# Performance work log

Hardware: AMD Instinct MI355X
Metric: run time of the kernel (lower is better)

## Reference

```python
import jax, jax.numpy as jnp
import numpy as np

B, C, H, W, D = 1, 128, 64, 64, 64
CQ = C // 8


def setup_inputs() -> dict:
    key = jax.random.key(0)
    ks = jax.random.split(key, 6)
    s = 0.05
    return {
        "x": jax.random.normal(ks[0], (B, C, H, W, D), jnp.float32),
        "y": jax.random.normal(ks[1], (B, C, H, W, D), jnp.float32),
        "Wq": jax.random.normal(ks[2], (CQ, C), jnp.float32) * s,
        "bq": jnp.zeros((CQ,), jnp.float32),
        "Wk": jax.random.normal(ks[3], (CQ, C), jnp.float32) * s,
        "bk": jnp.zeros((CQ,), jnp.float32),
        "Wv": jax.random.normal(ks[4], (C, C), jnp.float32) * s,
        "bv": jnp.zeros((C,), jnp.float32),
        # torch inits gamma to 0 (kills all attention grads); use a nonzero value
        "gamma": jax.random.normal(ks[5], (1,), jnp.float32),
    }


def _conv1x1(x, Wt, b):
    # 1x1x1 Conv3d == per-voxel linear over channels
    return jnp.einsum('bchwd,oc->bohwd', x, Wt) + b[None, :, None, None, None]


def _criss_cross(x, y, Wq, bq, Wk, bk, Wv, bv, gamma):
    Bs, Cs, Hs, Ws, Ds = x.shape
    Cq = Wq.shape[0]
    q = _conv1x1(x, Wq, bq)  # [B,Cq,H,W,D]
    k = _conv1x1(y, Wk, bk)  # [B,Cq,H,W,D]
    v = _conv1x1(x, Wv, bv)  # [B,C ,H,W,D]

    # exact transliteration of the torch permute/contiguous/view sequence
    qH = q.transpose(0, 3, 4, 1, 2).reshape(Bs * Ws * Ds, Cq, Hs).transpose(0, 2, 1)
    qW = q.transpose(0, 2, 4, 1, 3).reshape(Bs * Hs * Ds, Cq, Ws).transpose(0, 2, 1)
    qD = q.transpose(0, 2, 3, 1, 4).reshape(Bs * Hs * Ws, Cq, Ds).transpose(0, 2, 1)
    kH = k.transpose(0, 3, 4, 1, 2).reshape(Bs * Ws * Ds, Cq, Hs)
    kW = k.transpose(0, 2, 4, 1, 3).reshape(Bs * Hs * Ds, Cq, Ws)
    kD = k.transpose(0, 2, 3, 1, 4).reshape(Bs * Hs * Ws, Cq, Ds)
    vH = v.transpose(0, 3, 4, 1, 2).reshape(Bs * Ws * Ds, Cs, Hs)
    vW = v.transpose(0, 2, 4, 1, 3).reshape(Bs * Hs * Ds, Cs, Ws)
    vD = v.transpose(0, 2, 3, 1, 4).reshape(Bs * Hs * Ws, Cs, Ds)

    # INF(): -inf on the HxH diagonal, broadcast over the B*W*D batch
    inf_mask = jnp.where(jnp.eye(Hs, dtype=bool), -jnp.inf, 0.0)[None].astype(x.dtype)

    energy_H = (jnp.matmul(qH, kH) + inf_mask).reshape(Bs, Ws, Hs, Ds, Hs).transpose(0, 2, 1, 3, 4)
    energy_W = jnp.matmul(qW, kW).reshape(Bs, Hs, Ws, Ds, Ws)
    energy_D = jnp.matmul(qD, kD).reshape(Bs, Hs, Ws, Ds, Ds)

    # NOTE: original uses Softmax(dim=3) on the 5D concat -> softmax over the D axis
    concate = jax.nn.softmax(jnp.concatenate([energy_H, energy_W, energy_D], axis=4), axis=3)

    att_H = concate[..., 0:Hs].transpose(0, 2, 1, 3, 4).reshape(Bs * Ws * Ds, Hs, Hs)
    att_W = concate[..., Hs:Hs + Ws].reshape(Bs * Hs * Ds, Ws, Ws)
    att_D = concate[..., Hs + Ws:Hs + Ws + Ds].reshape(Bs * Hs * Ws, Ds, Ds)

    out_H = jnp.matmul(vH, att_H.transpose(0, 2, 1)).reshape(Bs, Ws, Cs, Hs, Ds).transpose(0, 2, 3, 1, 4)
    out_W = jnp.matmul(vW, att_W.transpose(0, 2, 1)).reshape(Bs, Hs, Cs, Ws, Ds).transpose(0, 2, 1, 3, 4)
    out_D = jnp.matmul(vD, att_D.transpose(0, 2, 1)).reshape(Bs, Hs, Cs, Ws, Ds).transpose(0, 2, 1, 3, 4)

    return gamma[0] * (out_H + out_W + out_D) + x


def reference(x, y, Wq, bq, Wk, bk, Wv, bv, gamma):
    return _criss_cross(x, y, Wq, bq, Wk, bk, Wv, bv, gamma)
```

## Files before the change

kernel.cpp:

```cpp
#include <hip/hip_runtime.h>

#define HWD 262144
#define WD  4096

typedef unsigned short bf16_t;
typedef unsigned short u16;
struct __align__(8) us4 { unsigned short x, y, z, w; };

typedef __bf16 bf16x8 __attribute__((ext_vector_type(8)));
typedef float  f32x4  __attribute__((ext_vector_type(4)));

__device__ inline float b2f(unsigned short u) {
    return __uint_as_float(((unsigned int)u) << 16);
}
__device__ inline unsigned short f2b(float f) {
    unsigned int u = __float_as_uint(f);
    u += 0x7fff + ((u >> 16) & 1);
    return (unsigned short)(u >> 16);
}

union FragU { us4 h[2]; bf16x8 v; };
__device__ inline bf16x8 ld8_a8(const u16* p) {
    FragU f; f.h[0] = *(const us4*)p; f.h[1] = *(const us4*)(p + 4); return f.v;
}
__device__ inline bf16x8 ld8_a16(const u16* p) {
    return *(const bf16x8*)p;
}

struct HL { bf16x8 h, l; };
__device__ inline HL split8(const float* w8) {
    FragU H, L;
    unsigned short hh[8], ll[8];
#pragma unroll
    for (int t = 0; t < 8; ++t) {
        hh[t] = f2b(w8[t]);
        ll[t] = f2b(w8[t] - b2f(hh[t]));
    }
    H.h[0].x = hh[0]; H.h[0].y = hh[1]; H.h[0].z = hh[2]; H.h[0].w = hh[3];
    H.h[1].x = hh[4]; H.h[1].y = hh[5]; H.h[1].z = hh[6]; H.h[1].w = hh[7];
    L.h[0].x = ll[0]; L.h[0].y = ll[1]; L.h[0].z = ll[2]; L.h[0].w = ll[3];
    L.h[1].x = ll[4]; L.h[1].y = ll[5]; L.h[1].z = ll[6]; L.h[1].w = ll[7];
    HL r; r.h = H.v; r.l = L.v; return r;
}

__global__ __launch_bounds__(512, 4) void conv_v_mfma(
    const float* __restrict__ x, const float* __restrict__ Wv,
    const float* __restrict__ bv, bf16_t* __restrict__ v)
{
    __shared__ __align__(16) u16 Xh[64][136];
    __shared__ __align__(16) u16 Xl[64][136];
    const int tid  = threadIdx.x;
    const int lane = tid & 63;
    const int wv   = tid >> 6;
    const int lg = lane >> 4, lr = lane & 15;
    const int n0 = blockIdx.x * 64;

    const int m0 = wv * 16;
    bf16x8 Ah[4], Al[4];
#pragma unroll
    for (int ks = 0; ks < 4; ++ks) {
        float w8[8];
        const float* wp = &Wv[(m0 + lr) * 128 + ks * 32 + lg * 8];
        *(float4*)&w8[0] = *(const float4*)wp;
        *(float4*)&w8[4] = *(const float4*)(wp + 4);
        HL hl = split8(w8);
        Ah[ks] = hl.h; Al[ks] = hl.l;
    }

#pragma unroll
    for (int gi = 0; gi < 2; ++gi) {
        const int g = wv + gi * 8;
        float v8[8];
#pragma unroll
        for (int s = 0; s < 8; ++s)
            v8[s] = x[(size_t)(g * 8 + s) * HWD + n0 + lane];
        HL hl = split8(v8);
        *(bf16x8*)&Xh[lane][g * 8] = hl.h;
        *(bf16x8*)&Xl[lane][g * 8] = hl.l;
    }
    __syncthreads();

    f32x4 acc[4];
#pragma unroll
    for (int ns = 0; ns < 4; ++ns) acc[ns] = (f32x4){0.f, 0.f, 0.f, 0.f};
#pragma unroll
    for (int ks = 0; ks < 4; ++ks) {
#pragma unroll
        for (int ns = 0; ns < 4; ++ns) {
            const bf16x8 Bh = ld8_a16(&Xh[ns * 16 + lr][ks * 32 + lg * 8]);
            const bf16x8 Bl = ld8_a16(&Xl[ns * 16 + lr][ks * 32 + lg * 8]);
            acc[ns] = __builtin_amdgcn_mfma_f32_16x16x32_bf16(Ah[ks], Bh, acc[ns], 0, 0, 0);
            acc[ns] = __builtin_amdgcn_mfma_f32_16x16x32_bf16(Ah[ks], Bl, acc[ns], 0, 0, 0);
            acc[ns] = __builtin_amdgcn_mfma_f32_16x16x32_bf16(Al[ks], Bh, acc[ns], 0, 0, 0);
        }
    }
#pragma unroll
    for (int ns = 0; ns < 4; ++ns)
#pragma unroll
        for (int r = 0; r < 4; ++r) {
            const int m = m0 + 4 * lg + r;
            v[(size_t)m * HWD + n0 + ns * 16 + lr] = f2b(acc[ns][r] + bv[m]);
        }
}

__global__ __launch_bounds__(256, 4) void conv_qk_mfma(
    const float* __restrict__ x, const float* __restrict__ y,
    const float* __restrict__ Wq, const float* __restrict__ bq,
    const float* __restrict__ Wk, const float* __restrict__ bk,
    bf16_t* __restrict__ q, bf16_t* __restrict__ k)
{
    __shared__ __align__(16) u16 Sh[2][32][136];
    __shared__ __align__(16) u16 Sl[2][32][136];
    const int tid  = threadIdx.x;
    const int lane = tid & 63;
    const int wv   = tid >> 6;
    const int lg = lane >> 4, lr = lane & 15;
    const int n0 = blockIdx.x * 32;

    const float* W    = (wv < 2) ? Wq : Wk;
    const float* bias = (wv < 2) ? bq : bk;
    bf16_t*      dst  = (wv < 2) ? q  : k;
    bf16x8 Ah[4], Al[4];
#pragma unroll
    for (int ks = 0; ks < 4; ++ks) {
        float w8[8];
        const float* wp = &W[lr * 128 + ks * 32 + lg * 8];
        *(float4*)&w8[0] = *(const float4*)wp;
        *(float4*)&w8[4] = *(const float4*)(wp + 4);
        HL hl = split8(w8);
        Ah[ks] = hl.h; Al[ks] = hl.l;
    }

    {
        const int n  = tid & 31;
        const int kb = (tid >> 5) * 16;
#pragma unroll
        for (int a = 0; a < 2; ++a) {
            const float* src = a ? y : x;
#pragma unroll
            for (int gg = 0; gg < 2; ++gg) {
                float v8[8];
#pragma unroll
                for (int s = 0; s < 8; ++s)
                    v8[s] = src[(size_t)(kb + gg * 8 + s) * HWD + n0 + n];
                HL hl = split8(v8);
                *(bf16x8*)&Sh[a][n][kb + gg * 8] = hl.h;
                *(bf16x8*)&Sl[a][n][kb + gg * 8] = hl.l;
            }
        }
    }
    __syncthreads();

    const int a  = wv >> 1;
    const int ns = wv & 1;
    f32x4 acc = (f32x4){0.f, 0.f, 0.f, 0.f};
#pragma unroll
    for (int ks = 0; ks < 4; ++ks) {
        const bf16x8 Bh = ld8_a16(&Sh[a][ns * 16 + lr][ks * 32 + lg * 8]);
        const bf16x8 Bl = ld8_a16(&Sl[a][ns * 16 + lr][ks * 32 + lg * 8]);
        acc = __builtin_amdgcn_mfma_f32_16x16x32_bf16(Ah[ks], Bh, acc, 0, 0, 0);
        acc = __builtin_amdgcn_mfma_f32_16x16x32_bf16(Ah[ks], Bl, acc, 0, 0, 0);
        acc = __builtin_amdgcn_mfma_f32_16x16x32_bf16(Al[ks], Bh, acc, 0, 0, 0);
    }
#pragma unroll
    for (int r = 0; r < 4; ++r) {
        const int m = 4 * lg + r;
        dst[(size_t)m * HWD + n0 + ns * 16 + lr] = f2b(acc[r] + bias[m]);
    }
}

__global__ __launch_bounds__(256) void t_wd_kernel(
    const bf16_t* __restrict__ src, bf16_t* __restrict__ dst)
{
    const int h = blockIdx.x, c = blockIdx.y;
    __shared__ bf16_t tile[64][68];
    const size_t base = (size_t)c * HWD + h * WD;
    const int tid = threadIdx.x;
#pragma unroll
    for (int i = 0; i < 4; ++i) {
        const int f = (tid + i * 256) * 4;
        const int w = f >> 6, d = f & 63;
        const us4 val = *(const us4*)&src[base + w * 64 + d];
        tile[w][d] = val.x; tile[w][d + 1] = val.y;
        tile[w][d + 2] = val.z; tile[w][d + 3] = val.w;
    }
    __syncthreads();
#pragma unroll
    for (int i = 0; i < 4; ++i) {
        const int f = (tid + i * 256) * 4;
        const int d = f >> 6, w0 = f & 63;
        us4 o; o.x = tile[w0][d]; o.y = tile[w0 + 1][d];
        o.z = tile[w0 + 2][d]; o.w = tile[w0 + 3][d];
        *(us4*)&dst[base + d * 64 + w0] = o;
    }
}

__global__ __launch_bounds__(256) void t_hd_kernel(
    const bf16_t* __restrict__ src, bf16_t* __restrict__ dst)
{
    const int w = blockIdx.x, c = blockIdx.y;
    __shared__ bf16_t tile[64][68];
    const size_t cb = (size_t)c * HWD;
    const int tid = threadIdx.x;
#pragma unroll
    for (int i = 0; i < 4; ++i) {
        const int f = (tid + i * 256) * 4;
        const int h = f >> 6, d0 = f & 63;
        const us4 val = *(const us4*)&src[cb + h * WD + w * 64 + d0];
        tile[h][d0] = val.x; tile[h][d0 + 1] = val.y;
        tile[h][d0 + 2] = val.z; tile[h][d0 + 3] = val.w;
    }
    __syncthreads();
#pragma unroll
    for (int i = 0; i < 4; ++i) {
        const int f = (tid + i * 256) * 4;
        const int d = f >> 6, h0 = f & 63;
        us4 o; o.x = tile[h0][d]; o.y = tile[h0 + 1][d];
        o.z = tile[h0 + 2][d]; o.w = tile[h0 + 3][d];
        *(us4*)&dst[cb + w * WD + d * 64 + h0] = o;
    }
}

template<bool MASK>
__device__ __forceinline__ void cc_phase(
    const u16* __restrict__ qp, const u16* __restrict__ kp,
    const u16* __restrict__ vp, const size_t base, const int tid,
    u16 (*Qt)[36], u16 (*Kt)[36], u16 (*Vs)[72],
    float (*EA)[68], u16 (*PB)[72], float (*red)[64], f32x4* acc)
{
    const int w  = tid >> 6;
    const int l  = tid & 63;
    const int lg = l >> 4, lr = l & 15;

    __syncthreads();
    us4 vreg[8];
#pragma unroll
    for (int i = 0; i < 8; ++i) {
        const int f = (tid + i * 256) * 4;
        vreg[i] = *(const us4*)&vp[(size_t)(f >> 6) * HWD + base + (f & 63)];
    }
    {
        const int j = tid & 63, c0 = (tid >> 6) * 4;
        const size_t gb = base + j;
        us4 qv, kv;
        qv.x = qp[(size_t)(c0 + 0) * HWD + gb];
        qv.y = qp[(size_t)(c0 + 1) * HWD + gb];
        qv.z = qp[(size_t)(c0 + 2) * HWD + gb];
        qv.w = qp[(size_t)(c0 + 3) * HWD + gb];
        kv.x = kp[(size_t)(c0 + 0) * HWD + gb];
        kv.y = kp[(size_t)(c0 + 1) * HWD + gb];
        kv.z = kp[(size_t)(c0 + 2) * HWD + gb];
        kv.w = kp[(size_t)(c0 + 3) * HWD + gb];
        *(us4*)&Qt[j][c0] = qv;
        *(us4*)&Kt[j][c0] = kv;
    }
    __syncthreads();
    {
        const bf16x8 bk = ld8_a8(&Kt[16 * w + lr][8 * lg]);
#pragma unroll
        for (int ti = 0; ti < 4; ++ti) {
            const bf16x8 aq = ld8_a8(&Qt[16 * ti + lr][8 * lg]);
            f32x4 e = {0.f, 0.f, 0.f, 0.f};
            e = __builtin_amdgcn_mfma_f32_16x16x32_bf16(aq, bk, e, 0, 0, 0);
#pragma unroll
            for (int r = 0; r < 4; ++r)
                EA[16 * ti + 4 * lg + r][16 * w + lr] = e[r];
        }
    }
    __syncthreads();
    {
        const int j = tid & 63, seg = tid >> 6;
        float vals[16];
        float m = -1e30f;
#pragma unroll
        for (int i = 0; i < 16; ++i) {
            float vv = EA[seg * 16 + i][j];
            if (MASK && (seg * 16 + i) == j) vv = -1e30f;
            vals[i] = vv; m = fmaxf(m, vv);
        }
        red[seg][j] = m;
        __syncthreads();
        m = fmaxf(fmaxf(red[0][j], red[1][j]), fmaxf(red[2][j], red[3][j]));
        float ss = 0.f;
#pragma unroll
        for (int i = 0; i < 16; ++i) { vals[i] = __expf(vals[i] - m); ss += vals[i]; }
        __syncthreads();
        red[seg][j] = ss;
        __syncthreads();
        ss = red[0][j] + red[1][j] + red[2][j] + red[3][j];
        const float inv = 1.f / ss;
        const int odd = j & 1;
#pragma unroll
        for (int ii = 0; ii < 8; ++ii) {
            const float plo = vals[ii] * inv;
            const float phi = vals[8 + ii] * inv;
            const float olo = __shfl_xor(plo, 1);
            const float ohi = __shfl_xor(phi, 1);
            const int   i   = odd ? 8 + ii : ii;
            const float a   = odd ? ohi : plo;
            const float b   = odd ? phi : olo;
            const unsigned pk = (unsigned)f2b(a) | ((unsigned)f2b(b) << 16);
            *(unsigned*)&PB[seg * 16 + i][j & ~1] = pk;
        }
    }
#pragma unroll
    for (int i = 0; i < 8; ++i) {
        const int f = (tid + i * 256) * 4;
        *(us4*)&Vs[f >> 6][f & 63] = vreg[i];
    }
    __syncthreads();
#pragma unroll
    for (int ks = 0; ks < 2; ++ks) {
        const bf16x8 bp = ld8_a16(&PB[16 * w + lr][32 * ks + 8 * lg]);
#pragma unroll
        for (int tm = 0; tm < 8; ++tm) {
            const bf16x8 av = ld8_a16(&Vs[16 * tm + lr][32 * ks + 8 * lg]);
            acc[tm] = __builtin_amdgcn_mfma_f32_16x16x32_bf16(av, bp, acc[tm], 0, 0, 0);
        }
    }
}

__global__ __launch_bounds__(256) void cc_wd_kernel(
    const bf16_t* __restrict__ q,  const bf16_t* __restrict__ k,
    const bf16_t* __restrict__ v,
    const bf16_t* __restrict__ qT, const bf16_t* __restrict__ kT,
    const bf16_t* __restrict__ vT,
    const float* __restrict__ x, const float* __restrict__ gamma,
    float* __restrict__ out)
{
    const int s   = blockIdx.x;
    const int hh  = blockIdx.y;
    const int tid = threadIdx.x;
    __shared__ __align__(16) u16 Qt[64][36];
    __shared__ __align__(16) u16 Kt[64][36];
    __shared__ __align__(16) u16 Vs[128][72];
    __shared__ __align__(16) float EA[64][68];
    __shared__ float red[4][64];
    u16 (*PB)[72] = (u16(*)[72])EA;
    f32x4 acc[8];
#pragma unroll
    for (int i = 0; i < 8; ++i) acc[i] = (f32x4){0.f, 0.f, 0.f, 0.f};
    {
        const int rr = tid >> 2, slot = tid & 3;
        us4 z; z.x = z.y = z.z = z.w = 0;
        *(us4*)&Qt[rr][16 + 4 * slot] = z;
        *(us4*)&Kt[rr][16 + 4 * slot] = z;
    }
    const size_t base = (size_t)hh * WD + s * 64;
    for (int phase = 0; phase < 2; ++phase) {
        const u16* qp = phase ? q : qT;
        const u16* kp = phase ? k : kT;
        const u16* vp = phase ? v : vT;
        cc_phase<false>(qp, kp, vp, base, tid, Qt, Kt, Vs, EA, PB, red, acc);
    }
    const int w = tid >> 6, l = tid & 63, lg = l >> 4, lr = l & 15;
    const int dd = 16 * w + lr;
    const float g = gamma[0];
#pragma unroll
    for (int tm = 0; tm < 8; ++tm)
#pragma unroll
        for (int r = 0; r < 4; ++r) {
            const int c = 16 * tm + 4 * lg + r;
            const size_t o = (size_t)(2 * s + (c >> 6)) * HWD +
                             (size_t)hh * WD + (size_t)(c & 63) * 64 + dd;
            out[o] = g * acc[tm][r] + x[o];
        }
}

__global__ __launch_bounds__(256) void cc_h_kernel(
    const bf16_t* __restrict__ qH, const bf16_t* __restrict__ kH,
    const bf16_t* __restrict__ vH,
    const float* __restrict__ gamma, float* __restrict__ out)
{
    const int t   = blockIdx.x;
    const int ww  = blockIdx.y;
    const int tid = threadIdx.x;
    __shared__ __align__(16) u16 Qt[64][36];
    __shared__ __align__(16) u16 Kt[64][36];
    __shared__ __align__(16) u16 Vs[128][72];
    __shared__ __align__(16) float EA[64][68];
    __shared__ float red[4][64];
    u16 (*PB)[72] = (u16(*)[72])EA;
    f32x4 acc[8];
#pragma unroll
    for (int i = 0; i < 8; ++i) acc[i] = (f32x4){0.f, 0.f, 0.f, 0.f};
    {
        const int rr = tid >> 2, slot = tid & 3;
        us4 z; z.x = z.y = z.z = z.w = 0;
        *(us4*)&Qt[rr][16 + 4 * slot] = z;
        *(us4*)&Kt[rr][16 + 4 * slot] = z;
    }
    const size_t base = (size_t)ww * WD + t * 64;
    cc_phase<true>(qH, kH, vH, base, tid, Qt, Kt, Vs, EA, PB, red, acc);

    const int w = tid >> 6, l = tid & 63, lg = l >> 4, lr = l & 15;
    const int dd = 16 * w + lr;
    const float g = gamma[0];
#pragma unroll
    for (int tm = 0; tm < 8; ++tm)
#pragma unroll
        for (int r = 0; r < 4; ++r) {
            const int c = 16 * tm + 4 * lg + r;
            const size_t o = (size_t)(2 * t + (c >> 6)) * HWD +
                             (size_t)(c & 63) * WD + (size_t)ww * 64 + dd;
            out[o] += g * acc[tm][r];
        }
}

extern "C" void kernel_launch(void* const* d_in, const int* in_sizes, int n_in,
                              void* d_out, int out_size, void* d_ws, size_t ws_size,
                              hipStream_t stream)
{
    const float* x     = (const float*)d_in[0];
    const float* y     = (const float*)d_in[1];
    const float* Wq    = (const float*)d_in[2];
    const float* bq    = (const float*)d_in[3];
    const float* Wk    = (const float*)d_in[4];
    const float* bk    = (const float*)d_in[5];
    const float* Wv    = (const float*)d_in[6];
    const float* bv    = (const float*)d_in[7];
    const float* gamma = (const float*)d_in[8];
    float* out = (float*)d_out;

    bf16_t* A0 = (bf16_t*)d_ws;
    bf16_t* v  = A0;
    bf16_t* q  = A0 + (size_t)128 * HWD;
    bf16_t* k  = A0 + (size_t)144 * HWD;
    bf16_t* A1 = A0 + (size_t)160 * HWD;
    bf16_t* A2 = A1 + (size_t)160 * HWD;

    conv_v_mfma  <<<4096, 512, 0, stream>>>(x, Wv, bv, v);
    conv_qk_mfma <<<8192, 256, 0, stream>>>(x, y, Wq, bq, Wk, bk, q, k);
    t_wd_kernel  <<<dim3(64, 160), 256, 0, stream>>>(A0, A1);
    t_hd_kernel  <<<dim3(64, 160), 256, 0, stream>>>(A0, A2);
    cc_wd_kernel <<<dim3(64, 64), 256, 0, stream>>>(
        q, k, v, A1 + (size_t)128 * HWD, A1 + (size_t)144 * HWD, A1, x, gamma, out);
    cc_h_kernel  <<<dim3(64, 64), 256, 0, stream>>>(
        A2 + (size_t)128 * HWD, A2 + (size_t)144 * HWD, A2, gamma, out);
}
```

Measured before the change: 574.9 us.

## Fuse q conv into v conv, prefetch both phases, alias Q/K LDS

The q projection now runs inside the v-projection kernel, reusing the same staged x tile so x is read once for both. The k projection becomes its own y-only kernel. The criss-cross kernels load the global q/k/v data for both phases into registers up front, overlapping global latency with compute. Q/K tiles are aliased into the V shared buffer with occupancy hints of 4 blocks. This trades register pressure (two prefetched phases) for lower LDS use and fewer redundant global reads.

```diff
diff --git a/kernel.cpp b/kernel.cpp
--- a/kernel.cpp
+++ b/kernel.cpp
@@ -43,9 +43,11 @@
     HL r; r.h = H.v; r.l = L.v; return r;
 }
 
-__global__ __launch_bounds__(512, 4) void conv_v_mfma(
+__global__ __launch_bounds__(512, 4) void conv_x_mfma(
     const float* __restrict__ x, const float* __restrict__ Wv,
-    const float* __restrict__ bv, bf16_t* __restrict__ v)
+    const float* __restrict__ bv, const float* __restrict__ Wq,
+    const float* __restrict__ bq,
+    bf16_t* __restrict__ v, bf16_t* __restrict__ q)
 {
     __shared__ __align__(16) u16 Xh[64][136];
     __shared__ __align__(16) u16 Xl[64][136];
@@ -54,9 +56,9 @@
     const int wv   = tid >> 6;
     const int lg = lane >> 4, lr = lane & 15;
     const int n0 = blockIdx.x * 64;
-
     const int m0 = wv * 16;
-    bf16x8 Ah[4], Al[4];
+
+    bf16x8 Ah[4], Al[4], Qh[4], Ql[4];
 #pragma unroll
     for (int ks = 0; ks < 4; ++ks) {
         float w8[8];
@@ -66,6 +68,17 @@
         HL hl = split8(w8);
         Ah[ks] = hl.h; Al[ks] = hl.l;
     }
+    if (wv < 4) {
+#pragma unroll
+        for (int ks = 0; ks < 4; ++ks) {
+            float w8[8];
+            const float* wp = &Wq[lr * 128 + ks * 32 + lg * 8];
+            *(float4*)&w8[0] = *(const float4*)wp;
+            *(float4*)&w8[4] = *(const float4*)(wp + 4);
+            HL hl = split8(w8);
+            Qh[ks] = hl.h; Ql[ks] = hl.l;
+        }
+    }
 
 #pragma unroll
     for (int gi = 0; gi < 2; ++gi) {
@@ -83,6 +96,7 @@
     f32x4 acc[4];
 #pragma unroll
     for (int ns = 0; ns < 4; ++ns) acc[ns] = (f32x4){0.f, 0.f, 0.f, 0.f};
+    f32x4 accq = (f32x4){0.f, 0.f, 0.f, 0.f};
 #pragma unroll
     for (int ks = 0; ks < 4; ++ks) {
 #pragma unroll
@@ -92,6 +106,11 @@
             acc[ns] = __builtin_amdgcn_mfma_f32_16x16x32_bf16(Ah[ks], Bh, acc[ns], 0, 0, 0);
             acc[ns] = __builtin_amdgcn_mfma_f32_16x16x32_bf16(Ah[ks], Bl, acc[ns], 0, 0, 0);
             acc[ns] = __builtin_amdgcn_mfma_f32_16x16x32_bf16(Al[ks], Bh, acc[ns], 0, 0, 0);
+            if (wv < 4 && ns == wv) {
+                accq = __builtin_amdgcn_mfma_f32_16x16x32_bf16(Qh[ks], Bh, accq, 0, 0, 0);
+                accq = __builtin_amdgcn_mfma_f32_16x16x32_bf16(Qh[ks], Bl, accq, 0, 0, 0);
+                accq = __builtin_amdgcn_mfma_f32_16x16x32_bf16(Ql[ks], Bh, accq, 0, 0, 0);
+            }
         }
     }
 #pragma unroll
@@ -101,63 +120,58 @@
             const int m = m0 + 4 * lg + r;
             v[(size_t)m * HWD + n0 + ns * 16 + lr] = f2b(acc[ns][r] + bv[m]);
         }
-}
-
-__global__ __launch_bounds__(256, 4) void conv_qk_mfma(
-    const float* __restrict__ x, const float* __restrict__ y,
-    const float* __restrict__ Wq, const float* __restrict__ bq,
-    const float* __restrict__ Wk, const float* __restrict__ bk,
-    bf16_t* __restrict__ q, bf16_t* __restrict__ k)
-{
-    __shared__ __align__(16) u16 Sh[2][32][136];
-    __shared__ __align__(16) u16 Sl[2][32][136];
+    if (wv < 4) {
+#pragma unroll
+        for (int r = 0; r < 4; ++r) {
+            const int m = 4 * lg + r;
+            q[(size_t)m * HWD + n0 + wv * 16 + lr] = f2b(accq[r] + bq[m]);
+        }
+    }
+}
+
+__global__ __launch_bounds__(256, 4) void conv_y_mfma(
+    const float* __restrict__ y, const float* __restrict__ Wk,
+    const float* __restrict__ bk, bf16_t* __restrict__ k)
+{
+    __shared__ __align__(16) u16 Yh[64][136];
+    __shared__ __align__(16) u16 Yl[64][136];
     const int tid  = threadIdx.x;
     const int lane = tid & 63;
     const int wv   = tid >> 6;
     const int lg = lane >> 4, lr = lane & 15;
-    const int n0 = blockIdx.x * 32;
-
-    const float* W    = (wv < 2) ? Wq : Wk;
-    const float* bias = (wv < 2) ? bq : bk;
-    bf16_t*      dst  = (wv < 2) ? q  : k;
+    const int n0 = blockIdx.x * 64;
+
     bf16x8 Ah[4], Al[4];
 #pragma unroll
     for (int ks = 0; ks < 4; ++ks) {
         float w8[8];
-        const float* wp = &W[lr * 128 + ks * 32 + lg * 8];
+        const float* wp = &Wk[lr * 128 + ks * 32 + lg * 8];
         *(float4*)&w8[0] = *(const float4*)wp;
         *(float4*)&w8[4] = *(const float4*)(wp + 4);
         HL hl = split8(w8);
         Ah[ks] = hl.h; Al[ks] = hl.l;
     }
-
     {
-        const int n  = tid & 31;
-        const int kb = (tid >> 5) * 16;
-#pragma unroll
-        for (int a = 0; a < 2; ++a) {
-            const float* src = a ? y : x;
-#pragma unroll
-            for (int gg = 0; gg < 2; ++gg) {
-                float v8[8];
-#pragma unroll
-                for (int s = 0; s < 8; ++s)
-                    v8[s] = src[(size_t)(kb + gg * 8 + s) * HWD + n0 + n];
-                HL hl = split8(v8);
-                *(bf16x8*)&Sh[a][n][kb + gg * 8] = hl.h;
-                *(bf16x8*)&Sl[a][n][kb + gg * 8] = hl.l;
-            }
-        }
-    }
-    __syncthreads();
-
-    const int a  = wv >> 1;
-    const int ns = wv & 1;
+        const int n = tid & 63;
+#pragma unroll
+        for (int gi = 0; gi < 4; ++gi) {
+            const int g = (tid >> 6) * 4 + gi;
+            float v8[8];
+#pragma unroll
+            for (int s = 0; s < 8; ++s)
+                v8[s] = y[(size_t)(g * 8 + s) * HWD + n0 + n];
+            HL hl = split8(v8);
+            *(bf16x8*)&Yh[n][g * 8] = hl.h;
+            *(bf16x8*)&Yl[n][g * 8] = hl.l;
+        }
+    }
+    __syncthreads();
+
     f32x4 acc = (f32x4){0.f, 0.f, 0.f, 0.f};
 #pragma unroll
     for (int ks = 0; ks < 4; ++ks) {
-        const bf16x8 Bh = ld8_a16(&Sh[a][ns * 16 + lr][ks * 32 + lg * 8]);
-        const bf16x8 Bl = ld8_a16(&Sl[a][ns * 16 + lr][ks * 32 + lg * 8]);
+        const bf16x8 Bh = ld8_a16(&Yh[wv * 16 + lr][ks * 32 + lg * 8]);
+        const bf16x8 Bl = ld8_a16(&Yl[wv * 16 + lr][ks * 32 + lg * 8]);
         acc = __builtin_amdgcn_mfma_f32_16x16x32_bf16(Ah[ks], Bh, acc, 0, 0, 0);
         acc = __builtin_amdgcn_mfma_f32_16x16x32_bf16(Ah[ks], Bl, acc, 0, 0, 0);
         acc = __builtin_amdgcn_mfma_f32_16x16x32_bf16(Al[ks], Bh, acc, 0, 0, 0);
@@ -165,7 +179,7 @@
 #pragma unroll
     for (int r = 0; r < 4; ++r) {
         const int m = 4 * lg + r;
-        dst[(size_t)m * HWD + n0 + ns * 16 + lr] = f2b(acc[r] + bias[m]);
+        k[(size_t)m * HWD + n0 + wv * 16 + lr] = f2b(acc[r] + bk[m]);
     }
 }
 
@@ -221,10 +235,32 @@
     }
 }
 
+struct PR { us4 vreg[8]; us4 qv, kv; };
+
+__device__ __forceinline__ void cc_load(
+    const u16* __restrict__ qp, const u16* __restrict__ kp,
+    const u16* __restrict__ vp, const size_t base, const int tid, PR& R)
+{
+#pragma unroll
+    for (int i = 0; i < 8; ++i) {
+        const int f = (tid + i * 256) * 4;
+        R.vreg[i] = *(const us4*)&vp[(size_t)(f >> 6) * HWD + base + (f & 63)];
+    }
+    const int c0 = (tid >> 6) * 4;
+    const size_t gb = base + (tid & 63);
+    R.qv.x = qp[(size_t)(c0 + 0) * HWD + gb];
+    R.qv.y = qp[(size_t)(c0 + 1) * HWD + gb];
+    R.qv.z = qp[(size_t)(c0 + 2) * HWD + gb];
+    R.qv.w = qp[(size_t)(c0 + 3) * HWD + gb];
+    R.kv.x = kp[(size_t)(c0 + 0) * HWD + gb];
+    R.kv.y = kp[(size_t)(c0 + 1) * HWD + gb];
+    R.kv.z = kp[(size_t)(c0 + 2) * HWD + gb];
+    R.kv.w = kp[(size_t)(c0 + 3) * HWD + gb];
+}
+
 template<bool MASK>
-__device__ __forceinline__ void cc_phase(
-    const u16* __restrict__ qp, const u16* __restrict__ kp,
-    const u16* __restrict__ vp, const size_t base, const int tid,
+__device__ __forceinline__ void cc_compute(
+    PR& R, const int tid,
     u16 (*Qt)[36], u16 (*Kt)[36], u16 (*Vs)[72],
     float (*EA)[68], u16 (*PB)[72], float (*red)[64], f32x4* acc)
 {
@@ -233,26 +269,13 @@
     const int lg = l >> 4, lr = l & 15;
 
     __syncthreads();
-    us4 vreg[8];
-#pragma unroll
-    for (int i = 0; i < 8; ++i) {
-        const int f = (tid + i * 256) * 4;
-        vreg[i] = *(const us4*)&vp[(size_t)(f >> 6) * HWD + base + (f & 63)];
-    }
     {
         const int j = tid & 63, c0 = (tid >> 6) * 4;
-        const size_t gb = base + j;
-        us4 qv, kv;
-        qv.x = qp[(size_t)(c0 + 0) * HWD + gb];
-        qv.y = qp[(size_t)(c0 + 1) * HWD + gb];
-        qv.z = qp[(size_t)(c0 + 2) * HWD + gb];
-        qv.w = qp[(size_t)(c0 + 3) * HWD + gb];
-        kv.x = kp[(size_t)(c0 + 0) * HWD + gb];
-        kv.y = kp[(size_t)(c0 + 1) * HWD + gb];
-        kv.z = kp[(size_t)(c0 + 2) * HWD + gb];
-        kv.w = kp[(size_t)(c0 + 3) * HWD + gb];
-        *(us4*)&Qt[j][c0] = qv;
-        *(us4*)&Kt[j][c0] = kv;
+        *(us4*)&Qt[j][c0] = R.qv;
+        *(us4*)&Kt[j][c0] = R.kv;
+        us4 z; z.x = z.y = z.z = z.w = 0;
+        *(us4*)&Qt[j][16 + c0] = z;
+        *(us4*)&Kt[j][16 + c0] = z;
     }
     __syncthreads();
     {
@@ -306,7 +329,7 @@
 #pragma unroll
     for (int i = 0; i < 8; ++i) {
         const int f = (tid + i * 256) * 4;
-        *(us4*)&Vs[f >> 6][f & 63] = vreg[i];
+        *(us4*)&Vs[f >> 6][f & 63] = R.vreg[i];
     }
     __syncthreads();
 #pragma unroll
@@ -320,7 +343,7 @@
     }
 }
 
-__global__ __launch_bounds__(256) void cc_wd_kernel(
+__global__ __launch_bounds__(256, 4) void cc_wd_kernel(
     const bf16_t* __restrict__ q,  const bf16_t* __restrict__ k,
     const bf16_t* __restrict__ v,
     const bf16_t* __restrict__ qT, const bf16_t* __restrict__ kT,
@@ -331,28 +354,24 @@
     const int s   = blockIdx.x;
     const int hh  = blockIdx.y;
     const int tid = threadIdx.x;
-    __shared__ __align__(16) u16 Qt[64][36];
-    __shared__ __align__(16) u16 Kt[64][36];
-    __shared__ __align__(16) u16 Vs[128][72];
+    __shared__ __align__(16) u16 VsU[128][72];
     __shared__ __align__(16) float EA[64][68];
     __shared__ float red[4][64];
+    u16 (*Qt)[36] = (u16(*)[36])&VsU[0][0];
+    u16 (*Kt)[36] = (u16(*)[36])((u16*)&VsU[0][0] + 64 * 36);
+    u16 (*Vs)[72] = VsU;
     u16 (*PB)[72] = (u16(*)[72])EA;
     f32x4 acc[8];
 #pragma unroll
     for (int i = 0; i < 8; ++i) acc[i] = (f32x4){0.f, 0.f, 0.f, 0.f};
-    {
-        const int rr = tid >> 2, slot = tid & 3;
-        us4 z; z.x = z.y = z.z = z.w = 0;
-        *(us4*)&Qt[rr][16 + 4 * slot] = z;
-        *(us4*)&Kt[rr][16 + 4 * slot] = z;
-    }
+
     const size_t base = (size_t)hh * WD + s * 64;
-    for (int phase = 0; phase < 2; ++phase) {
-        const u16* qp = phase ? q : qT;
-        const u16* kp = phase ? k : kT;
-        const u16* vp = phase ? v : vT;
-        cc_phase<false>(qp, kp, vp, base, tid, Qt, Kt, Vs, EA, PB, red, acc);
-    }
+    PR R0, R1;
+    cc_load(qT, kT, vT, base, tid, R0);
+    cc_load(q,  k,  v,  base, tid, R1);
+    cc_compute<false>(R0, tid, Qt, Kt, Vs, EA, PB, red, acc);
+    cc_compute<false>(R1, tid, Qt, Kt, Vs, EA, PB, red, acc);
+
     const int w = tid >> 6, l = tid & 63, lg = l >> 4, lr = l & 15;
     const int dd = 16 * w + lr;
     const float g = gamma[0];
@@ -367,7 +386,7 @@
         }
 }
 
-__global__ __launch_bounds__(256) void cc_h_kernel(
+__global__ __launch_bounds__(256, 4) void cc_h_kernel(
     const bf16_t* __restrict__ qH, const bf16_t* __restrict__ kH,
     const bf16_t* __restrict__ vH,
     const float* __restrict__ gamma, float* __restrict__ out)
@@ -375,23 +394,21 @@
     const int t   = blockIdx.x;
     const int ww  = blockIdx.y;
     const int tid = threadIdx.x;
-    __shared__ __align__(16) u16 Qt[64][36];
-    __shared__ __align__(16) u16 Kt[64][36];
-    __shared__ __align__(16) u16 Vs[128][72];
+    __shared__ __align__(16) u16 VsU[128][72];
     __shared__ __align__(16) float EA[64][68];
     __shared__ float red[4][64];
+    u16 (*Qt)[36] = (u16(*)[36])&VsU[0][0];
+    u16 (*Kt)[36] = (u16(*)[36])((u16*)&VsU[0][0] + 64 * 36);
+    u16 (*Vs)[72] = VsU;
     u16 (*PB)[72] = (u16(*)[72])EA;
     f32x4 acc[8];
 #pragma unroll
     for (int i = 0; i < 8; ++i) acc[i] = (f32x4){0.f, 0.f, 0.f, 0.f};
-    {
-        const int rr = tid >> 2, slot = tid & 3;
-        us4 z; z.x = z.y = z.z = z.w = 0;
-        *(us4*)&Qt[rr][16 + 4 * slot] = z;
-        *(us4*)&Kt[rr][16 + 4 * slot] = z;
-    }
+
     const size_t base = (size_t)ww * WD + t * 64;
-    cc_phase<true>(qH, kH, vH, base, tid, Qt, Kt, Vs, EA, PB, red, acc);
+    PR R;
+    cc_load(qH, kH, vH, base, tid, R);
+    cc_compute<true>(R, tid, Qt, Kt, Vs, EA, PB, red, acc);
 
     const int w = tid >> 6, l = tid & 63, lg = l >> 4, lr = l & 15;
     const int dd = 16 * w + lr;
@@ -429,12 +446,12 @@
     bf16_t* A1 = A0 + (size_t)160 * HWD;
     bf16_t* A2 = A1 + (size_t)160 * HWD;
 
-    conv_v_mfma  <<<4096, 512, 0, stream>>>(x, Wv, bv, v);
-    conv_qk_mfma <<<8192, 256, 0, stream>>>(x, y, Wq, bq, Wk, bk, q, k);
-    t_wd_kernel  <<<dim3(64, 160), 256, 0, stream>>>(A0, A1);
-    t_hd_kernel  <<<dim3(64, 160), 256, 0, stream>>>(A0, A2);
-    cc_wd_kernel <<<dim3(64, 64), 256, 0, stream>>>(
+    conv_x_mfma <<<4096, 512, 0, stream>>>(x, Wv, bv, Wq, bq, v, q);
+    conv_y_mfma <<<4096, 256, 0, stream>>>(y, Wk, bk, k);
+    t_wd_kernel <<<dim3(64, 160), 256, 0, stream>>>(A0, A1);
+    t_hd_kernel <<<dim3(64, 160), 256, 0, stream>>>(A0, A2);
+    cc_wd_kernel<<<dim3(64, 64), 256, 0, stream>>>(
         q, k, v, A1 + (size_t)128 * HWD, A1 + (size_t)144 * HWD, A1, x, gamma, out);
-    cc_h_kernel  <<<dim3(64, 64), 256, 0, stream>>>(
+    cc_h_kernel <<<dim3(64, 64), 256, 0, stream>>>(
         A2 + (size_t)128 * HWD, A2 + (size_t)144 * HWD, A2, gamma, out);
 }
```

Measured after the change: 622.7 us. 1.08x slower.
